# Kernel tuning notes

Hardware: AMD Instinct MI355X
Metric: run time of the kernel (lower is better)

Reference implementation:

```python
import jax, jax.numpy as jnp
import numpy as np
from jax.scipy.special import gammainc, gammaln

M, N, D, L, J = 64, 2048, 256, 64, 384  # queries, train points, feat dim, buckets, ncx2 series terms
SIGMA2 = 4.0          # sigma=2.0
BUCKET_SHRINK = 1.0
NEG = -999999.0


def _make_buckets():
    # Mirrors fit(): linspace(ncx2.ppf(1e-4, D*shrink, 0), ncx2.ppf(1-1e-4, D, D*shrink/sigma2)) * sigma2,
    # using the normal approximation to the (non)central chi-square quantiles (scipy unavailable).
    z = 3.7190165  # Phi^{-1}(0.9999)
    df = float(D)
    nc0 = df * BUCKET_SHRINK / SIGMA2
    lb = df * BUCKET_SHRINK - z * np.sqrt(2.0 * df * BUCKET_SHRINK)
    ub = (df + nc0) + z * np.sqrt(2.0 * (df + 2.0 * nc0))
    return jnp.asarray(np.linspace(lb, ub, L) * SIGMA2, dtype=jnp.float32)


def setup_inputs() -> dict:
    key = jax.random.key(0)
    k1, k2, k3 = jax.random.split(key, 3)
    X = jax.random.normal(k1, (M, D), dtype=jnp.float32)
    train_X = jax.random.normal(k2, (N, D), dtype=jnp.float32)
    train_y = jax.random.randint(k3, (N,), 0, 2, dtype=jnp.int32)
    buckets = _make_buckets()
    return {"X": X, "train_X": train_X, "buckets": buckets, "train_y": train_y}


def _ncx2_cdf_matrix(nc, buckets):
    # ncx2.cdf(x, df=D, nc) = sum_j Pois(nc/2)[j] * gammainc(D/2 + j, x/2)
    # nc: [M, N]; buckets are the (already /sigma2) CDF evaluation points x: [L]
    half_nc = nc * 0.5                                            # [M, N]
    j = jnp.arange(J, dtype=jnp.float32)                          # [J]
    logw = (-half_nc[..., None] + j * jnp.log(half_nc)[..., None]
            - gammaln(j + 1.0))                                   # [M, N, J]
    w = jnp.exp(logw)
    G = gammainc(0.5 * D + j[:, None], 0.5 * buckets[None, :])    # [J, L]
    return jnp.einsum('mnj,jl->mnl', w, G)                        # [M, N, L]


def _predict(X, train_X, buckets, train_y):
    # squared euclidean distances, [M, N]
    dists = (jnp.sum(X * X, -1)[:, None] + jnp.sum(train_X * train_X, -1)[None, :]
             - 2.0 * (X @ train_X.T))
    dists = jnp.maximum(dists, 0.0)
    F = _ncx2_cdf_matrix(dists / SIGMA2, buckets / SIGMA2)        # [M, N, L]
    p_mat = jnp.concatenate([F[..., 1:] - F[..., :-1], 1.0 - F[..., -1:]], axis=-1)  # [M, N, L]
    psum = jnp.cumsum(p_mat[..., ::-1], axis=-1)[..., ::-1]       # reverse cumsum over buckets
    logpprod = jnp.cumsum(jnp.log(jnp.maximum(psum, 1e-30)), axis=1)  # scan over train points
    logpprod = jnp.maximum(logpprod, NEG)
    logpprod = jnp.where(jnp.isnan(logpprod), NEG, logpprod)
    # term1[i, l] = logpprod[i-1, l+1] (0 for i==0; NEG at l==L-1 for i>0)
    inner = logpprod[:, :-1, 1:]                                  # [M, N-1, L-1]
    term1 = jnp.concatenate([inner, jnp.full((M, N - 1, 1), NEG, dtype=inner.dtype)], axis=-1)
    term1 = jnp.concatenate([jnp.zeros((M, 1, L), dtype=inner.dtype), term1], axis=1)  # [M, N, L]
    term2 = logpprod[:, -1:, :] - logpprod                        # [M, N, L]
    p = jnp.sum(p_mat * jnp.exp(term1 + term2), axis=-1)          # [M, N] per-point KNN prob
    onehot = jax.nn.one_hot(train_y, 2, dtype=p.dtype)            # [N, 2]
    pred = p @ onehot                                             # [M, 2]
    return pred / jnp.sum(pred, axis=-1, keepdims=True)


def reference(X, train_X, buckets, train_y):
    return _predict(X, train_X, buckets, train_y)
```

## Files before the change

### kernel.cpp

```cpp
#include <hip/hip_runtime.h>
#include <math.h>

#define M_ 64
#define N_ 2048
#define D_ 256
#define L_ 64
#define J_ 384
#define CHUNKS 32
#define CN 64

typedef _Float16 half8 __attribute__((ext_vector_type(8)));
typedef float f32x4 __attribute__((ext_vector_type(4)));

#define OFF_F16   0u
#define OFF_LG8   49152u
#define OFF_INV   49344u
#define OFF_SQX   50880u
#define OFF_PRED  51136u
#define OFF_DIST  51712u
#define OFF_CHUNK 576000u
#define OFF_TOT   1624576u
#define OFF_PSUM  1657344u

__global__ __launch_bounds__(512)
void k_setup(const float* __restrict__ buckets, const float* __restrict__ Xg,
             char* __restrict__ ws) {
    _Float16* F16 = (_Float16*)(ws + OFF_F16);
    float* lg8  = (float*)(ws + OFF_LG8);
    float* invt = (float*)(ws + OFF_INV);
    float* sqX  = (float*)(ws + OFF_SQX);
    float* pred = (float*)(ws + OFF_PRED);
    int t = threadIdx.x;
    if (t < 64) {
        double x = (double)buckets[t] * 0.125;
        const double a0 = 128.0;
        double gln = lgamma(a0);
        double q;
        if (x < a0 + 1.0) {
            double ap = a0, sum = 1.0 / a0, del = sum;
            for (int it = 0; it < 4000; ++it) {
                ap += 1.0; del *= x / ap; sum += del;
                if (fabs(del) < fabs(sum) * 1e-17) break;
            }
            q = 1.0 - sum * exp(-x + a0 * log(x) - gln);
        } else {
            double b = x + 1.0 - a0, c = 1e300, d = 1.0 / b, h = d;
            for (int i = 1; i <= 4000; ++i) {
                double an = -(double)i * ((double)i - a0);
                b += 2.0;
                d = an * d + b; if (fabs(d) < 1e-300) d = 1e-300;
                c = b + an / c; if (fabs(c) < 1e-300) c = 1e-300;
                d = 1.0 / d;
                double delc = d * c; h *= delc;
                if (fabs(delc - 1.0) < 1e-16) break;
            }
            q = exp(-x + a0 * log(x) - gln) * h;
        }
        double tt = exp(a0 * log(x) - x - lgamma(a0 + 1.0));
        for (int j = 0; j < J_; ++j) {
            double F = 1.0 - q;
            if (F < 0.0) F = 0.0;
            F16[t * J_ + j] = (_Float16)F;
            q += tt; if (q > 1.0) q = 1.0;
            tt *= x / (a0 + (double)j + 1.0);
        }
    } else if (t < 128) {
        int i = t - 64;
        const float4* xr = (const float4*)(Xg + i * D_);
        float s0 = 0, s1 = 0, s2 = 0, s3 = 0;
        for (int k = 0; k < D_ / 4; ++k) {
            float4 v = xr[k];
            s0 = fmaf(v.x, v.x, s0); s1 = fmaf(v.y, v.y, s1);
            s2 = fmaf(v.z, v.z, s2); s3 = fmaf(v.w, v.w, s3);
        }
        sqX[i] = (s0 + s1) + (s2 + s3);
        if (i < 48) lg8[i] = (float)lgamma(8.0 * (double)i + 1.0);
        else { int p = i - 48; for (int e = 0; e < 8; ++e) pred[8 * p + e] = 0.f; }
    } else {
        int i = t - 128;
        invt[i] = 1.0f / (float)(i + 1);
    }
}

__global__ __launch_bounds__(256)
void k_dist(const float* __restrict__ Xg, const float* __restrict__ TXg,
            char* __restrict__ ws) {
    const float* sqX = (const float*)(ws + OFF_SQX);
    float* dist      = (float*)(ws + OFF_DIST);
    int bid = blockIdx.x;
    int n  = ((bid & 7) << 8) + threadIdx.x;
    int mg = (bid >> 3) << 2;
    const float4* T4 = (const float4*)(TXg + (size_t)n * D_);
    const float4* X4 = (const float4*)Xg;
    float4 a0{0,0,0,0}, a1{0,0,0,0}, a2{0,0,0,0}, a3{0,0,0,0}, st{0,0,0,0};
#pragma unroll 8
    for (int k = 0; k < D_ / 4; ++k) {
        float4 tv = T4[k];
        st.x = fmaf(tv.x, tv.x, st.x); st.y = fmaf(tv.y, tv.y, st.y);
        st.z = fmaf(tv.z, tv.z, st.z); st.w = fmaf(tv.w, tv.w, st.w);
        float4 x0 = X4[(mg + 0) * 64 + k];
        a0.x = fmaf(x0.x, tv.x, a0.x); a0.y = fmaf(x0.y, tv.y, a0.y);
        a0.z = fmaf(x0.z, tv.z, a0.z); a0.w = fmaf(x0.w, tv.w, a0.w);
        float4 x1 = X4[(mg + 1) * 64 + k];
        a1.x = fmaf(x1.x, tv.x, a1.x); a1.y = fmaf(x1.y, tv.y, a1.y);
        a1.z = fmaf(x1.z, tv.z, a1.z); a1.w = fmaf(x1.w, tv.w, a1.w);
        float4 x2 = X4[(mg + 2) * 64 + k];
        a2.x = fmaf(x2.x, tv.x, a2.x); a2.y = fmaf(x2.y, tv.y, a2.y);
        a2.z = fmaf(x2.z, tv.z, a2.z); a2.w = fmaf(x2.w, tv.w, a2.w);
        float4 x3 = X4[(mg + 3) * 64 + k];
        a3.x = fmaf(x3.x, tv.x, a3.x); a3.y = fmaf(x3.y, tv.y, a3.y);
        a3.z = fmaf(x3.z, tv.z, a3.z); a3.w = fmaf(x3.w, tv.w, a3.w);
    }
    float stt = (st.x + st.y) + (st.z + st.w);
    float d0 = (a0.x + a0.y) + (a0.z + a0.w);
    float d1 = (a1.x + a1.y) + (a1.z + a1.w);
    float d2 = (a2.x + a2.y) + (a2.z + a2.w);
    float d3 = (a3.x + a3.y) + (a3.z + a3.w);
    dist[(mg + 0) * N_ + n] = fmaxf(sqX[mg + 0] + stt - 2.f * d0, 0.f);
    dist[(mg + 1) * N_ + n] = fmaxf(sqX[mg + 1] + stt - 2.f * d1, 0.f);
    dist[(mg + 2) * N_ + n] = fmaxf(sqX[mg + 2] + stt - 2.f * d2, 0.f);
    dist[(mg + 3) * N_ + n] = fmaxf(sqX[mg + 3] + stt - 2.f * d3, 0.f);
}

__global__ __launch_bounds__(128)
void k_mfma(char* __restrict__ ws) {
    const float* dist     = (const float*)(ws + OFF_DIST);
    const _Float16* F16   = (const _Float16*)(ws + OFF_F16);
    const float* lg8      = (const float*)(ws + OFF_LG8);
    const float* invt     = (const float*)(ws + OFF_INV);
    float* psum           = (float*)(ws + OFF_PSUM);
    double* chunk         = (double*)(ws + OFF_CHUNK);

    __shared__ double s_part[2][64];

    int bid = blockIdx.x;
    int m = bid >> 5, c = bid & 31;
    int n0 = c << 6;
    int t = threadIdx.x;
    int w = t >> 6, l = t & 63;
    int col = l & 15, g = l >> 4;
    int rbase = n0 + (w << 5);

    const float* drow = dist + (m << 11);
    float la0 = drow[rbase + col];
    float la1 = drow[rbase + 16 + col];
    la0 *= 0.125f; la1 *= 0.125f;
    float ll0 = __logf(la0), ll1 = __logf(la1);

    f32x4 acc00 = {0,0,0,0}, acc01 = {0,0,0,0}, acc02 = {0,0,0,0}, acc03 = {0,0,0,0};
    f32x4 acc10 = {0,0,0,0}, acc11 = {0,0,0,0}, acc12 = {0,0,0,0}, acc13 = {0,0,0,0};

    for (int s = 0; s < 12; ++s) {
        int jb = (s << 5) + (g << 3);
        float jbf = (float)jb;
        half8 b0 = *(const half8*)(F16 + (size_t)(col     ) * J_ + jb);
        half8 b1 = *(const half8*)(F16 + (size_t)(col + 16) * J_ + jb);
        half8 b2 = *(const half8*)(F16 + (size_t)(col + 32) * J_ + jb);
        half8 b3 = *(const half8*)(F16 + (size_t)(col + 48) * J_ + jb);
        float lgv = lg8[(s << 2) + g];
        float4 iv0 = *(const float4*)(invt + jb);
        float4 iv1 = *(const float4*)(invt + jb + 4);
        {
            float wv = __expf(fmaf(jbf, ll0, -la0 - lgv));
            half8 a;
            a[0] = (_Float16)wv;
            wv *= la0 * iv0.x; a[1] = (_Float16)wv;
            wv *= la0 * iv0.y; a[2] = (_Float16)wv;
            wv *= la0 * iv0.z; a[3] = (_Float16)wv;
            wv *= la0 * iv0.w; a[4] = (_Float16)wv;
            wv *= la0 * iv1.x; a[5] = (_Float16)wv;
            wv *= la0 * iv1.y; a[6] = (_Float16)wv;
            wv *= la0 * iv1.z; a[7] = (_Float16)wv;
            acc00 = __builtin_amdgcn_mfma_f32_16x16x32_f16(a, b0, acc00, 0, 0, 0);
            acc01 = __builtin_amdgcn_mfma_f32_16x16x32_f16(a, b1, acc01, 0, 0, 0);
            acc02 = __builtin_amdgcn_mfma_f32_16x16x32_f16(a, b2, acc02, 0, 0, 0);
            acc03 = __builtin_amdgcn_mfma_f32_16x16x32_f16(a, b3, acc03, 0, 0, 0);
        }
        {
            float wv = __expf(fmaf(jbf, ll1, -la1 - lgv));
            half8 a;
            a[0] = (_Float16)wv;
            wv *= la1 * iv0.x; a[1] = (_Float16)wv;
            wv *= la1 * iv0.y; a[2] = (_Float16)wv;
            wv *= la1 * iv0.z; a[3] = (_Float16)wv;
            wv *= la1 * iv0.w; a[4] = (_Float16)wv;
            wv *= la1 * iv1.x; a[5] = (_Float16)wv;
            wv *= la1 * iv1.y; a[6] = (_Float16)wv;
            wv *= la1 * iv1.z; a[7] = (_Float16)wv;
            acc10 = __builtin_amdgcn_mfma_f32_16x16x32_f16(a, b0, acc10, 0, 0, 0);
            acc11 = __builtin_amdgcn_mfma_f32_16x16x32_f16(a, b1, acc11, 0, 0, 0);
            acc12 = __builtin_amdgcn_mfma_f32_16x16x32_f16(a, b2, acc12, 0, 0, 0);
            acc13 = __builtin_amdgcn_mfma_f32_16x16x32_f16(a, b3, acc13, 0, 0, 0);
        }
    }

    double lsum0 = 0.0, lsum1 = 0.0, lsum2 = 0.0, lsum3 = 0.0;
    float* pbase = psum + (((size_t)(m << 11) + rbase) << 6);
#define EPI(ACC, SP, TI, LS)                                                    \
    {                                                                           \
        _Pragma("unroll")                                                       \
        for (int r = 0; r < 4; ++r) {                                           \
            float ps = 1.f - (ACC)[r];                                          \
            int row = (SP) * 16 + g * 4 + r;                                    \
            pbase[((size_t)row << 6) + (TI) * 16 + col] = ps;                   \
            LS += (double)__logf(fmaxf(ps, 1e-30f));                            \
        }                                                                       \
    }
    EPI(acc00, 0, 0, lsum0) EPI(acc01, 0, 1, lsum1) EPI(acc02, 0, 2, lsum2) EPI(acc03, 0, 3, lsum3)
    EPI(acc10, 1, 0, lsum0) EPI(acc11, 1, 1, lsum1) EPI(acc12, 1, 2, lsum2) EPI(acc13, 1, 3, lsum3)
#undef EPI
    lsum0 += __shfl_xor(lsum0, 16); lsum0 += __shfl_xor(lsum0, 32);
    lsum1 += __shfl_xor(lsum1, 16); lsum1 += __shfl_xor(lsum1, 32);
    lsum2 += __shfl_xor(lsum2, 16); lsum2 += __shfl_xor(lsum2, 32);
    lsum3 += __shfl_xor(lsum3, 16); lsum3 += __shfl_xor(lsum3, 32);
    if (g == 0) {
        s_part[w][col]      = lsum0;
        s_part[w][16 + col] = lsum1;
        s_part[w][32 + col] = lsum2;
        s_part[w][48 + col] = lsum3;
    }
    __syncthreads();
    if (t < 64)
        chunk[((m << 5) + c) * 64 + t] = s_part[0][t] + s_part[1][t];
}

__global__ __launch_bounds__(256)
void k_prefix(char* __restrict__ ws) {
    double* chunks = (double*)(ws + OFF_CHUNK);
    double* tot    = (double*)(ws + OFF_TOT);
    int idx = blockIdx.x * 256 + threadIdx.x;
    int m = idx >> 6, l = idx & 63;
    double s = 0.0;
    for (int c = 0; c < CHUNKS; ++c) {
        int slot = (m * CHUNKS + c) * 64 + l;
        double v = chunks[slot];
        chunks[slot] = s;
        s += v;
    }
    tot[m * 64 + l] = s;
}

__global__ __launch_bounds__(64)
void k_scan(const int* __restrict__ ty, char* __restrict__ ws) {
    const float* psum  = (const float*)(ws + OFF_PSUM);
    const double* offs = (const double*)(ws + OFF_CHUNK);
    const double* tot  = (const double*)(ws + OFF_TOT);
    float* pred        = (float*)(ws + OFF_PRED);
    int b = blockIdx.x, m = b >> 5, c = b & (CHUNKS - 1), l = threadIdx.x;

    double cum = offs[(m * CHUNKS + c) * 64 + l];
    double T   = tot[m * 64 + l];
    const float* P = psum + (((size_t)m * N_ + (size_t)c * CN) << 6);
    int n0 = c * CN;
    float a0 = 0.f, a1 = 0.f;
    for (int i = 0; i < CN; ++i) {
        float pv = P[((size_t)i << 6) + l];
        float lv = __logf(fmaxf(pv, 1e-30f));
        double nbr = __shfl_down(cum, 1);
        float pvn  = __shfl_down(pv, 1);
        double cin = cum + (double)lv;
        int n = n0 + i;
        double t1 = (n == 0) ? 0.0 : ((l == 63) ? -999999.0 : nbr);
        double t2 = T - cin;
        float e = (float)(t1 + t2);
        float pm = (l == 63) ? pv : (pv - pvn);
        float contrib = pm * __expf(e);
        int y = ty[n];
        a0 += (y == 0) ? contrib : 0.f;
        a1 += (y == 1) ? contrib : 0.f;
        cum = cin;
    }
#pragma unroll
    for (int o = 32; o > 0; o >>= 1) {
        a0 += __shfl_down(a0, o);
        a1 += __shfl_down(a1, o);
    }
    if (l == 0) {
        atomicAdd(&pred[m * 2 + 0], a0);
        atomicAdd(&pred[m * 2 + 1], a1);
    }
}

__global__ __launch_bounds__(64)
void k_norm(char* __restrict__ ws, float* __restrict__ out) {
    const float* pred = (const float*)(ws + OFF_PRED);
    int m = threadIdx.x;
    float a = pred[2 * m], b = pred[2 * m + 1];
    float s = a + b;
    out[2 * m]     = a / s;
    out[2 * m + 1] = b / s;
}

extern "C" void kernel_launch(void* const* d_in, const int* in_sizes, int n_in,
                              void* d_out, int out_size, void* d_ws, size_t ws_size,
                              hipStream_t stream) {
    const float* X       = (const float*)d_in[0];
    const float* train_X = (const float*)d_in[1];
    const float* buckets = (const float*)d_in[2];
    const int*   train_y = (const int*)d_in[3];
    float* out = (float*)d_out;
    char*  ws  = (char*)d_ws;

    k_setup<<<1, 512, 0, stream>>>(buckets, X, ws);
    k_dist<<<128, 256, 0, stream>>>(X, train_X, ws);
    k_mfma<<<M_ * CHUNKS, 128, 0, stream>>>(ws);
    k_prefix<<<(M_ * 64) / 256, 256, 0, stream>>>(ws);
    k_scan<<<M_ * CHUNKS, 64, 0, stream>>>(train_y, ws);
    k_norm<<<1, 64, 0, stream>>>(ws, out);
}
```

Measured before the change: 203.7 us.

## Parallelize gamma table setup, fuse distance into MFMA kernel, drop prefix kernel

The serial single-thread gammainc table build is split across 12 blocks, each starting its own incomplete-gamma evaluation at a = 128+32*jg, which shortens the serial dependency chain. The distance computation is folded into the MFMA kernel: each block computes its 64 distances into shared memory, so the separate dist kernel and its global round trip go away. The chunk prefix kernel is removed and each scan block recomputes its own prefix and total from the chunk sums. Together this cuts two launches, at the cost of recomputing the train-point norms 64 times (once per query) and redundantly reading chunk sums in every scan block.

```diff
diff --git a/kernel.cpp b/kernel.cpp
--- a/kernel.cpp
+++ b/kernel.cpp
@@ -17,36 +17,35 @@
 #define OFF_INV   49344u
 #define OFF_SQX   50880u
 #define OFF_PRED  51136u
-#define OFF_DIST  51712u
 #define OFF_CHUNK 576000u
-#define OFF_TOT   1624576u
 #define OFF_PSUM  1657344u
 
-__global__ __launch_bounds__(512)
-void k_setup(const float* __restrict__ buckets, const float* __restrict__ Xg,
-             char* __restrict__ ws) {
+__global__ __launch_bounds__(64)
+void k_tab(const float* __restrict__ buckets, const float* __restrict__ Xg,
+           char* __restrict__ ws) {
     _Float16* F16 = (_Float16*)(ws + OFF_F16);
     float* lg8  = (float*)(ws + OFF_LG8);
     float* invt = (float*)(ws + OFF_INV);
     float* sqX  = (float*)(ws + OFF_SQX);
     float* pred = (float*)(ws + OFF_PRED);
-    int t = threadIdx.x;
-    if (t < 64) {
-        double x = (double)buckets[t] * 0.125;
-        const double a0 = 128.0;
-        double gln = lgamma(a0);
+    int jg = blockIdx.x, l = threadIdx.x;
+
+    if (jg < 12) {
+        double x = (double)buckets[l] * 0.125;
+        double a = 128.0 + 32.0 * (double)jg;
+        double gln = lgamma(a);
         double q;
-        if (x < a0 + 1.0) {
-            double ap = a0, sum = 1.0 / a0, del = sum;
-            for (int it = 0; it < 4000; ++it) {
+        if (x < a + 1.0) {
+            double ap = a, sum = 1.0 / a, del = sum;
+            for (int it = 0; it < 3000; ++it) {
                 ap += 1.0; del *= x / ap; sum += del;
-                if (fabs(del) < fabs(sum) * 1e-17) break;
+                if (fabs(del) < fabs(sum) * 1e-16) break;
             }
-            q = 1.0 - sum * exp(-x + a0 * log(x) - gln);
+            q = 1.0 - sum * exp(-x + a * log(x) - gln);
         } else {
-            double b = x + 1.0 - a0, c = 1e300, d = 1.0 / b, h = d;
-            for (int i = 1; i <= 4000; ++i) {
-                double an = -(double)i * ((double)i - a0);
+            double b = x + 1.0 - a, c = 1e300, d = 1.0 / b, h = d;
+            for (int i = 1; i <= 3000; ++i) {
+                double an = -(double)i * ((double)i - a);
                 b += 2.0;
                 d = an * d + b; if (fabs(d) < 1e-300) d = 1e-300;
                 c = b + an / c; if (fabs(c) < 1e-300) c = 1e-300;
@@ -54,97 +53,77 @@
                 double delc = d * c; h *= delc;
                 if (fabs(delc - 1.0) < 1e-16) break;
             }
-            q = exp(-x + a0 * log(x) - gln) * h;
-        }
-        double tt = exp(a0 * log(x) - x - lgamma(a0 + 1.0));
-        for (int j = 0; j < J_; ++j) {
+            q = exp(-x + a * log(x) - gln) * h;
+        }
+        double tt = exp(a * log(x) - x - lgamma(a + 1.0));
+        for (int jj = 0; jj < 32; ++jj) {
             double F = 1.0 - q;
             if (F < 0.0) F = 0.0;
-            F16[t * J_ + j] = (_Float16)F;
+            F16[l * J_ + (jg << 5) + jj] = (_Float16)F;
             q += tt; if (q > 1.0) q = 1.0;
-            tt *= x / (a0 + (double)j + 1.0);
-        }
-    } else if (t < 128) {
-        int i = t - 64;
-        const float4* xr = (const float4*)(Xg + i * D_);
+            tt *= x / (a + (double)jj + 1.0);
+        }
+    } else {
+        const float4* xr = (const float4*)(Xg + l * D_);
         float s0 = 0, s1 = 0, s2 = 0, s3 = 0;
         for (int k = 0; k < D_ / 4; ++k) {
             float4 v = xr[k];
             s0 = fmaf(v.x, v.x, s0); s1 = fmaf(v.y, v.y, s1);
             s2 = fmaf(v.z, v.z, s2); s3 = fmaf(v.w, v.w, s3);
         }
-        sqX[i] = (s0 + s1) + (s2 + s3);
-        if (i < 48) lg8[i] = (float)lgamma(8.0 * (double)i + 1.0);
-        else { int p = i - 48; for (int e = 0; e < 8; ++e) pred[8 * p + e] = 0.f; }
-    } else {
-        int i = t - 128;
-        invt[i] = 1.0f / (float)(i + 1);
-    }
-}
-
-__global__ __launch_bounds__(256)
-void k_dist(const float* __restrict__ Xg, const float* __restrict__ TXg,
-            char* __restrict__ ws) {
-    const float* sqX = (const float*)(ws + OFF_SQX);
-    float* dist      = (float*)(ws + OFF_DIST);
-    int bid = blockIdx.x;
-    int n  = ((bid & 7) << 8) + threadIdx.x;
-    int mg = (bid >> 3) << 2;
-    const float4* T4 = (const float4*)(TXg + (size_t)n * D_);
-    const float4* X4 = (const float4*)Xg;
-    float4 a0{0,0,0,0}, a1{0,0,0,0}, a2{0,0,0,0}, a3{0,0,0,0}, st{0,0,0,0};
-#pragma unroll 8
-    for (int k = 0; k < D_ / 4; ++k) {
-        float4 tv = T4[k];
-        st.x = fmaf(tv.x, tv.x, st.x); st.y = fmaf(tv.y, tv.y, st.y);
-        st.z = fmaf(tv.z, tv.z, st.z); st.w = fmaf(tv.w, tv.w, st.w);
-        float4 x0 = X4[(mg + 0) * 64 + k];
-        a0.x = fmaf(x0.x, tv.x, a0.x); a0.y = fmaf(x0.y, tv.y, a0.y);
-        a0.z = fmaf(x0.z, tv.z, a0.z); a0.w = fmaf(x0.w, tv.w, a0.w);
-        float4 x1 = X4[(mg + 1) * 64 + k];
-        a1.x = fmaf(x1.x, tv.x, a1.x); a1.y = fmaf(x1.y, tv.y, a1.y);
-        a1.z = fmaf(x1.z, tv.z, a1.z); a1.w = fmaf(x1.w, tv.w, a1.w);
-        float4 x2 = X4[(mg + 2) * 64 + k];
-        a2.x = fmaf(x2.x, tv.x, a2.x); a2.y = fmaf(x2.y, tv.y, a2.y);
-        a2.z = fmaf(x2.z, tv.z, a2.z); a2.w = fmaf(x2.w, tv.w, a2.w);
-        float4 x3 = X4[(mg + 3) * 64 + k];
-        a3.x = fmaf(x3.x, tv.x, a3.x); a3.y = fmaf(x3.y, tv.y, a3.y);
-        a3.z = fmaf(x3.z, tv.z, a3.z); a3.w = fmaf(x3.w, tv.w, a3.w);
-    }
-    float stt = (st.x + st.y) + (st.z + st.w);
-    float d0 = (a0.x + a0.y) + (a0.z + a0.w);
-    float d1 = (a1.x + a1.y) + (a1.z + a1.w);
-    float d2 = (a2.x + a2.y) + (a2.z + a2.w);
-    float d3 = (a3.x + a3.y) + (a3.z + a3.w);
-    dist[(mg + 0) * N_ + n] = fmaxf(sqX[mg + 0] + stt - 2.f * d0, 0.f);
-    dist[(mg + 1) * N_ + n] = fmaxf(sqX[mg + 1] + stt - 2.f * d1, 0.f);
-    dist[(mg + 2) * N_ + n] = fmaxf(sqX[mg + 2] + stt - 2.f * d2, 0.f);
-    dist[(mg + 3) * N_ + n] = fmaxf(sqX[mg + 3] + stt - 2.f * d3, 0.f);
+        sqX[l] = (s0 + s1) + (s2 + s3);
+        if (l < 48) lg8[l] = (float)lgamma(8.0 * (double)l + 1.0);
+        for (int i = l; i < J_; i += 64) invt[i] = 1.0f / (float)(i + 1);
+        pred[2 * l] = 0.f; pred[2 * l + 1] = 0.f;
+    }
 }
 
 __global__ __launch_bounds__(128)
-void k_mfma(char* __restrict__ ws) {
-    const float* dist     = (const float*)(ws + OFF_DIST);
-    const _Float16* F16   = (const _Float16*)(ws + OFF_F16);
-    const float* lg8      = (const float*)(ws + OFF_LG8);
-    const float* invt     = (const float*)(ws + OFF_INV);
-    float* psum           = (float*)(ws + OFF_PSUM);
-    double* chunk         = (double*)(ws + OFF_CHUNK);
-
+void k_fused(const float* __restrict__ Xg, const float* __restrict__ TXg,
+             char* __restrict__ ws) {
+    const _Float16* F16 = (const _Float16*)(ws + OFF_F16);
+    const float* lg8    = (const float*)(ws + OFF_LG8);
+    const float* invt   = (const float*)(ws + OFF_INV);
+    const float* sqX    = (const float*)(ws + OFF_SQX);
+    float* psum         = (float*)(ws + OFF_PSUM);
+    double* chunk       = (double*)(ws + OFF_CHUNK);
+
+    __shared__ float  s_dist[64];
     __shared__ double s_part[2][64];
 
     int bid = blockIdx.x;
     int m = bid >> 5, c = bid & 31;
     int n0 = c << 6;
     int t = threadIdx.x;
+
+    {
+        int nloc = t >> 1, half = t & 1;
+        const float4* T4 = (const float4*)(TXg + (size_t)(n0 + nloc) * D_ + (half << 7));
+        const float4* X4 = (const float4*)(Xg + m * D_ + (half << 7));
+        float4 dd{0,0,0,0}, ss{0,0,0,0};
+#pragma unroll 8
+        for (int k = 0; k < 32; ++k) {
+            float4 tv = T4[k], xv = X4[k];
+            dd.x = fmaf(xv.x, tv.x, dd.x); dd.y = fmaf(xv.y, tv.y, dd.y);
+            dd.z = fmaf(xv.z, tv.z, dd.z); dd.w = fmaf(xv.w, tv.w, dd.w);
+            ss.x = fmaf(tv.x, tv.x, ss.x); ss.y = fmaf(tv.y, tv.y, ss.y);
+            ss.z = fmaf(tv.z, tv.z, ss.z); ss.w = fmaf(tv.w, tv.w, ss.w);
+        }
+        float dot = (dd.x + dd.y) + (dd.z + dd.w);
+        float st  = (ss.x + ss.y) + (ss.z + ss.w);
+        dot += __shfl_xor(dot, 1);
+        st  += __shfl_xor(st, 1);
+        if (half == 0)
+            s_dist[nloc] = fmaxf(sqX[m] + st - 2.f * dot, 0.f);
+    }
+    __syncthreads();
+
     int w = t >> 6, l = t & 63;
     int col = l & 15, g = l >> 4;
     int rbase = n0 + (w << 5);
 
-    const float* drow = dist + (m << 11);
-    float la0 = drow[rbase + col];
-    float la1 = drow[rbase + 16 + col];
-    la0 *= 0.125f; la1 *= 0.125f;
+    float la0 = s_dist[(w << 5) + col]      * 0.125f;
+    float la1 = s_dist[(w << 5) + 16 + col] * 0.125f;
     float ll0 = __logf(la0), ll1 = __logf(la1);
 
     f32x4 acc00 = {0,0,0,0}, acc01 = {0,0,0,0}, acc02 = {0,0,0,0}, acc03 = {0,0,0,0};
@@ -224,32 +203,20 @@
         chunk[((m << 5) + c) * 64 + t] = s_part[0][t] + s_part[1][t];
 }
 
-__global__ __launch_bounds__(256)
-void k_prefix(char* __restrict__ ws) {
-    double* chunks = (double*)(ws + OFF_CHUNK);
-    double* tot    = (double*)(ws + OFF_TOT);
-    int idx = blockIdx.x * 256 + threadIdx.x;
-    int m = idx >> 6, l = idx & 63;
-    double s = 0.0;
-    for (int c = 0; c < CHUNKS; ++c) {
-        int slot = (m * CHUNKS + c) * 64 + l;
-        double v = chunks[slot];
-        chunks[slot] = s;
-        s += v;
-    }
-    tot[m * 64 + l] = s;
-}
-
 __global__ __launch_bounds__(64)
 void k_scan(const int* __restrict__ ty, char* __restrict__ ws) {
-    const float* psum  = (const float*)(ws + OFF_PSUM);
-    const double* offs = (const double*)(ws + OFF_CHUNK);
-    const double* tot  = (const double*)(ws + OFF_TOT);
-    float* pred        = (float*)(ws + OFF_PRED);
+    const float* psum   = (const float*)(ws + OFF_PSUM);
+    const double* chunk = (const double*)(ws + OFF_CHUNK);
+    float* pred         = (float*)(ws + OFF_PRED);
     int b = blockIdx.x, m = b >> 5, c = b & (CHUNKS - 1), l = threadIdx.x;
 
-    double cum = offs[(m * CHUNKS + c) * 64 + l];
-    double T   = tot[m * 64 + l];
+    double cum = 0.0, T = 0.0;
+    for (int c2 = 0; c2 < CHUNKS; ++c2) {
+        double v = chunk[((m << 5) + c2) * 64 + l];
+        T += v;
+        if (c2 < c) cum += v;
+    }
+
     const float* P = psum + (((size_t)m * N_ + (size_t)c * CN) << 6);
     int n0 = c * CN;
     float a0 = 0.f, a1 = 0.f;
@@ -301,10 +268,8 @@
     float* out = (float*)d_out;
     char*  ws  = (char*)d_ws;
 
-    k_setup<<<1, 512, 0, stream>>>(buckets, X, ws);
-    k_dist<<<128, 256, 0, stream>>>(X, train_X, ws);
-    k_mfma<<<M_ * CHUNKS, 128, 0, stream>>>(ws);
-    k_prefix<<<(M_ * 64) / 256, 256, 0, stream>>>(ws);
+    k_tab<<<13, 64, 0, stream>>>(buckets, X, ws);
+    k_fused<<<M_ * CHUNKS, 128, 0, stream>>>(X, train_X, ws);
     k_scan<<<M_ * CHUNKS, 64, 0, stream>>>(train_y, ws);
     k_norm<<<1, 64, 0, stream>>>(ws, out);
 }
```

Result: faster. 168.1 us (-17.5%).
